# Optimization experiments

Measured on AMD Instinct MI355X. Metric: run time of the kernel, lower is better.

Reference implementation:

```python
import jax, jax.numpy as jnp
import numpy as np
import math

B, T, D, H = 4, 2048, 1024, 16
DH = D // H

def setup_inputs() -> dict:
    key = jax.random.key(0)
    ks = jax.random.split(key, 5)
    scale = 1.0 / math.sqrt(D)
    x = jax.random.normal(ks[0], (B, T, D), dtype=jnp.float32)
    Wq = jax.random.normal(ks[1], (D, D), dtype=jnp.float32) * scale
    Wk = jax.random.normal(ks[2], (D, D), dtype=jnp.float32) * scale
    Wv = jax.random.normal(ks[3], (D, D), dtype=jnp.float32) * scale
    Wo = jax.random.normal(ks[4], (D, D), dtype=jnp.float32) * scale
    mask = jnp.tril(jnp.ones((T, T), dtype=jnp.int32))  # causal, 1=keep
    return {"x": x, "mask": mask, "Wq": Wq, "Wk": Wk, "Wv": Wv, "Wo": Wo}

def reference(x, mask, Wq, Wk, Wv, Wo):
    Bx, Tx, Dx = x.shape
    # nn.Linear(bias=False): y = x @ W.T
    q = (x @ Wq.T).reshape(Bx, Tx, H, DH).transpose(0, 2, 1, 3)  # [B,H,T,dh]
    k = (x @ Wk.T).reshape(Bx, Tx, H, DH).transpose(0, 2, 1, 3)
    v = (x @ Wv.T).reshape(Bx, Tx, H, DH).transpose(0, 2, 1, 3)
    scores = jnp.einsum('bhqd,bhkd->bhqk', q, k) / math.sqrt(DH)
    m = mask[None, None, :, :]  # [1,1,T,T]
    scores = scores + (m == 0).astype(scores.dtype) * -1e9
    attn = jax.nn.softmax(scores, axis=-1)  # stable (max-subtract) like original
    out = jnp.einsum('bhqk,bhkd->bhqd', attn, v)
    out = out.transpose(0, 2, 1, 3).reshape(Bx, Tx, Dx)
    return out @ Wo.T
```

## Files before the change

kernel.cpp:

```cpp
#include <hip/hip_runtime.h>
#include <stdint.h>

#define B_  4
#define T_  2048
#define D_  1024
#define H_  16
#define DH_ 64

typedef unsigned short u16;
typedef __attribute__((ext_vector_type(8))) short bf16x8;
typedef __attribute__((ext_vector_type(8))) unsigned short u16x8;
typedef __attribute__((ext_vector_type(4))) unsigned short u16x4;
typedef __attribute__((ext_vector_type(4))) float f32x4;

#define NT_ ((size_t)B_ * T_ * D_)
#define QSCALE 0.18033688011112043f

__device__ __forceinline__ u16 f2bf(float f) {
    union { float f; uint32_t u; } v; v.f = f;
    uint32_t r = v.u + 0x7FFFu + ((v.u >> 16) & 1u);
    return (u16)(r >> 16);
}

__device__ __forceinline__ uint32_t pack2(float lo, float hi) {
    union { float f; uint32_t u; } a, b; a.f = lo; b.f = hi;
    return __builtin_amdgcn_perm(b.u, a.u, 0x07060302u);
}

__device__ __forceinline__ void gl2lds16(const u16* g, u16* l) {
    __builtin_amdgcn_global_load_lds(
        (const __attribute__((address_space(1))) unsigned int*)g,
        (__attribute__((address_space(3))) unsigned int*)l,
        16, 0, 0);
}

#define VMCNT(n) asm volatile("s_waitcnt vmcnt(" #n ")" ::: "memory")
#define SB0()    __builtin_amdgcn_sched_barrier(0)

__device__ __forceinline__ bf16x8 ldsrd(const u16* base, int row, int ks,
                                        int lq, int swzr) {
    int off = row * 128 + ks * 64 + lq * 16;
    return *(const bf16x8*)((const char*)base + (off ^ swzr));
}

__global__ __launch_bounds__(256) void cvt_x_kernel(
    const float* __restrict__ src, u16* __restrict__ dst, int n8)
{
    int i = blockIdx.x * 256 + threadIdx.x;
    if (i >= n8) return;
    f32x4 a = ((const f32x4*)src)[2 * i];
    f32x4 b = ((const f32x4*)src)[2 * i + 1];
    u16x8 o;
    o[0]=f2bf(a[0]); o[1]=f2bf(a[1]); o[2]=f2bf(a[2]); o[3]=f2bf(a[3]);
    o[4]=f2bf(b[0]); o[5]=f2bf(b[1]); o[6]=f2bf(b[2]); o[7]=f2bf(b[3]);
    ((u16x8*)dst)[i] = o;
}

__global__ __launch_bounds__(256) void cvt_w_kernel(
    const float* __restrict__ w0, const float* __restrict__ w1,
    const float* __restrict__ w2, const float* __restrict__ w3,
    u16* __restrict__ dst)
{
    const float* src = (blockIdx.y == 0) ? w0 : (blockIdx.y == 1) ? w1
                     : (blockIdx.y == 2) ? w2 : w3;
    u16* d = dst + (size_t)blockIdx.y * (D_ * D_);
    int i = blockIdx.x * 256 + threadIdx.x;
    f32x4 a = ((const f32x4*)src)[2 * i];
    f32x4 b = ((const f32x4*)src)[2 * i + 1];
    u16x8 o;
    o[0]=f2bf(a[0]); o[1]=f2bf(a[1]); o[2]=f2bf(a[2]); o[3]=f2bf(a[3]);
    o[4]=f2bf(b[0]); o[5]=f2bf(b[1]); o[6]=f2bf(b[2]); o[7]=f2bf(b[3]);
    ((u16x8*)d)[i] = o;
}

template<int OUT_MODE>
__global__ __launch_bounds__(512) void gemm8_kernel(
    const u16* __restrict__ X, const u16* __restrict__ W,
    void* __restrict__ C, int M, int N, int K)
{
    __shared__ __align__(16) u16 Ab2[2][256 * 64];
    __shared__ __align__(16) u16 Bb2[2][192 * 64];

    const int tid  = threadIdx.x;
    const int wave = tid >> 6;
    const int lane = tid & 63;
    const int lq = lane >> 4, lm = lane & 15;
    const int wm = wave >> 2;
    const int wn = wave & 3;

    const int xcd = (int)blockIdx.x & 7;
    const int idx = (int)blockIdx.x >> 3;
    const int m0 = (((xcd & 3) << 3) + (idx & 7)) << 8;
    const int n0 = (((xcd >> 2) << 3) + (idx >> 3)) * 192;

    const int srow = wave * 8 + (lane >> 3);
    const int scol = ((lane & 7) ^ (lane >> 3)) << 3;
    const u16* gA = X + (size_t)(m0 + srow) * K + scol;
    const u16* gB = W + (size_t)(n0 + srow) * K + scol;
    const size_t rK64 = (size_t)64 * K;

    const int swzr = (lm & 7) << 4;

    f32x4 acc[8][3] = {};
    bf16x8 afA[2][2], afB[2][2];
    bf16x8 bqA[3][2], bqB[3][2];
    const int NT = K >> 6;

    gl2lds16(gA,            (u16*)Ab2[0] + wave * 512);
    gl2lds16(gA + rK64,     (u16*)Ab2[0] + 4096  + wave * 512);
    gl2lds16(gA + 2 * rK64, (u16*)Ab2[0] + 8192  + wave * 512);
    gl2lds16(gA + 3 * rK64, (u16*)Ab2[0] + 12288 + wave * 512);
    gl2lds16(gB,            (u16*)Bb2[0] + wave * 512);
    gl2lds16(gB + rK64,     (u16*)Bb2[0] + 4096  + wave * 512);
    gl2lds16(gB + 2 * rK64, (u16*)Bb2[0] + 8192  + wave * 512);
    gl2lds16(gB + 64,            (u16*)Bb2[1] + wave * 512);
    gl2lds16(gB + 64 + rK64,     (u16*)Bb2[1] + 4096  + wave * 512);
    gl2lds16(gB + 64 + 2 * rK64, (u16*)Bb2[1] + 8192  + wave * 512);
    VMCNT(3);
    __builtin_amdgcn_s_barrier();
#pragma unroll
    for (int i2 = 0; i2 < 2; ++i2)
#pragma unroll
        for (int ks = 0; ks < 2; ++ks)
            afA[i2][ks] = ldsrd(Ab2[0], wm * 128 + i2 * 16 + lm, ks, lq, swzr);
#pragma unroll
    for (int j = 0; j < 3; ++j)
#pragma unroll
        for (int ks = 0; ks < 2; ++ks)
            bqA[j][ks] = ldsrd(Bb2[0], wn * 48 + j * 16 + lm, ks, lq, swzr);

    auto tile_body = [&](int t, bf16x8 (&bqU)[3][2], bf16x8 (&bqF)[3][2])
        __attribute__((always_inline)) -> void {
        const u16* Ac = Ab2[t & 1];
        const u16* An = Ab2[(t + 1) & 1];
        const u16* Bn = Bb2[(t + 1) & 1];
        u16* Abn = (u16*)Ab2[(t + 1) & 1];
        u16* Bbc = (u16*)Bb2[t & 1];
        const bool stA = (t + 1 < NT);
        const bool stB = (t + 2 < NT);
        const u16* gAs = gA + (size_t)(t + 1) * 64;
        const u16* gBs = gB + (size_t)(t + 2) * 64;

#define MFMA_PH(Q, AF, BQ)                                                  \
        __builtin_amdgcn_s_setprio(1);                                      \
        _Pragma("unroll")                                                   \
        for (int ks = 0; ks < 2; ++ks)                                      \
            _Pragma("unroll")                                               \
            for (int i2 = 0; i2 < 2; ++i2)                                  \
                _Pragma("unroll")                                           \
                for (int j = 0; j < 3; ++j)                                 \
                    acc[2 * (Q) + i2][j] =                                  \
                        __builtin_amdgcn_mfma_f32_16x16x32_bf16(            \
                            AF[i2][ks], BQ[j][ks], acc[2 * (Q) + i2][j],    \
                            0, 0, 0);                                       \
        __builtin_amdgcn_s_setprio(0);

#define RD_AF(SET, P, BASE)                                                 \
        _Pragma("unroll")                                                   \
        for (int i2 = 0; i2 < 2; ++i2)                                      \
            _Pragma("unroll")                                               \
            for (int ks = 0; ks < 2; ++ks)                                  \
                SET[i2][ks] = ldsrd(BASE,                                   \
                    wm * 128 + (2 * (P) + i2) * 16 + lm, ks, lq, swzr);

        RD_AF(afB, 1, Ac);
        if (stA) {
            gl2lds16(gAs,        Abn + wave * 512);
            gl2lds16(gAs + rK64, Abn + 4096 + wave * 512);
        }
        SB0(); __builtin_amdgcn_s_barrier(); SB0();
        MFMA_PH(0, afA, bqU); SB0();
        __builtin_amdgcn_s_barrier();

        RD_AF(afA, 2, Ac);
        if (stA) {
            gl2lds16(gAs + 2 * rK64, Abn + 8192  + wave * 512);
            gl2lds16(gAs + 3 * rK64, Abn + 12288 + wave * 512);
        }
        SB0(); __builtin_amdgcn_s_barrier(); SB0();
        MFMA_PH(1, afB, bqU); SB0();
        __builtin_amdgcn_s_barrier();

        RD_AF(afB, 3, Ac);
        if (stB) {
            gl2lds16(gBs,        Bbc + wave * 512);
            gl2lds16(gBs + rK64, Bbc + 4096 + wave * 512);
        }
        SB0(); __builtin_amdgcn_s_barrier(); SB0();
        MFMA_PH(2, afA, bqU); SB0();
        if (stB)      { VMCNT(2); }
        else if (stA) { VMCNT(0); }
        __builtin_amdgcn_s_barrier();

        if (stA) {
            RD_AF(afA, 0, An);
#pragma unroll
            for (int j = 0; j < 3; ++j)
#pragma unroll
                for (int ks = 0; ks < 2; ++ks)
                    bqF[j][ks] = ldsrd(Bn, wn * 48 + j * 16 + lm, ks, lq, swzr);
        }
        if (stB)
            gl2lds16(gBs + 2 * rK64, Bbc + 8192 + wave * 512);
        SB0(); __builtin_amdgcn_s_barrier(); SB0();
        MFMA_PH(3, afB, bqU); SB0();
        __builtin_amdgcn_s_barrier();
#undef RD_AF
#undef MFMA_PH
    };

#pragma unroll 1
    for (int tt = 0; tt < NT; tt += 2) {
        tile_body(tt,     bqA, bqB);
        tile_body(tt + 1, bqB, bqA);
    }

#pragma unroll
    for (int i = 0; i < 8; ++i)
#pragma unroll
        for (int j = 0; j < 3; ++j) {
            int rowb = m0 + wm * 128 + i * 16 + lq * 4;
            int col  = n0 + wn * 48 + j * 16 + lm;
            if (OUT_MODE == 2) {
#pragma unroll
                for (int r = 0; r < 4; ++r)
                    ((float*)C)[(size_t)(rowb + r) * N + col] = acc[i][j][r];
            } else {
                u16* Qp = (u16*)C;
                int region = col >> 10;
                int colr = col & 1023;
                if (region == 0) {
#pragma unroll
                    for (int r = 0; r < 4; ++r)
                        Qp[(size_t)(rowb + r) * D_ + colr] = f2bf(acc[i][j][r] * QSCALE);
                } else if (region == 1) {
#pragma unroll
                    for (int r = 0; r < 4; ++r)
                        (Qp + NT_)[(size_t)(rowb + r) * D_ + colr] = f2bf(acc[i][j][r]);
                } else {
                    int b = rowb >> 11, tt2 = rowb & (T_ - 1);
                    u16x4 pk;
#pragma unroll
                    for (int r = 0; r < 4; ++r) pk[r] = f2bf(acc[i][j][r]);
                    *(u16x4*)((Qp + 2 * NT_) + ((size_t)b * D_ + colr) * T_ + tt2) = pk;
                }
            }
        }
}

__global__ __launch_bounds__(256) void gemm_bt_kernel(
    const u16* __restrict__ X, const u16* __restrict__ W,
    float* __restrict__ C, int M, int N, int K)
{
    __shared__ __align__(16) u16 As[128 * 64];
    __shared__ __align__(16) u16 Bs[128 * 64];

    const int tid  = threadIdx.x;
    const int wave = tid >> 6;
    const int lane = tid & 63;
    const int lq = lane >> 4;
    const int lm = lane & 15;
    const int m0 = blockIdx.x * 128;
    const int n0 = blockIdx.y * 128;
    const int wm = (wave & 1) * 64;
    const int wn = (wave >> 1) * 64;

    f32x4 acc[4][4] = {};

    const int r0 = wave * 32 + (lane >> 3);
    const int c0 = (lane & 7) * 8;
    const u16* gA = X + (size_t)(m0 + r0) * K + c0;
    const u16* gB = W + (size_t)(n0 + r0) * K + c0;
    u16* lA = As + wave * 32 * 64;
    u16* lB = Bs + wave * 32 * 64;

    for (int k0 = 0; k0 < K; k0 += 64) {
#pragma unroll
        for (int p = 0; p < 4; ++p) {
            gl2lds16(gA + (size_t)p * 8 * K + k0, lA + p * 8 * 64);
            gl2lds16(gB + (size_t)p * 8 * K + k0, lB + p * 8 * 64);
        }
        __syncthreads();
#pragma unroll
        for (int ks = 0; ks < 2; ++ks) {
            bf16x8 af[4], bfr[4];
#pragma unroll
            for (int t = 0; t < 4; ++t)
                af[t] = *(const bf16x8*)(As + (wm + t * 16 + lm) * 64 + ks * 32 + lq * 8);
#pragma unroll
            for (int t = 0; t < 4; ++t)
                bfr[t] = *(const bf16x8*)(Bs + (wn + t * 16 + lm) * 64 + ks * 32 + lq * 8);
#pragma unroll
            for (int i = 0; i < 4; ++i)
#pragma unroll
                for (int j = 0; j < 4; ++j)
                    acc[i][j] = __builtin_amdgcn_mfma_f32_16x16x32_bf16(
                        af[i], bfr[j], acc[i][j], 0, 0, 0);
        }
        __syncthreads();
    }

#pragma unroll
    for (int i = 0; i < 4; ++i)
#pragma unroll
        for (int j = 0; j < 4; ++j) {
            int rowb = m0 + wm + i * 16 + lq * 4;
            int col  = n0 + wn + j * 16 + lm;
#pragma unroll
            for (int r = 0; r < 4; ++r)
                C[(size_t)(rowb + r) * N + col] = acc[i][j][r];
        }
}

__global__ __launch_bounds__(128) void attn_kernel(
    const u16* __restrict__ Qg, const u16* __restrict__ Kg,
    const u16* __restrict__ Vtg, u16* __restrict__ Og)
{
    __shared__ __align__(16) u16 Pl[2 * 64 * 40];

    const int tid  = threadIdx.x;
    const int wave = tid >> 6;
    const int lane = tid & 63;
    const int lq = lane >> 4, lm = lane & 15;
    const int id = blockIdx.x;
    const int xs = id & 7;
    const int bh = xs + 8 * ((id >> 3) & 7);
    const int qj = 31 - (id >> 6);
    const int b = bh >> 4, h = bh & 15;

    const size_t batchoff = (size_t)b * T_ * D_;
    const size_t headoff  = (size_t)h * DH_;
    const size_t vbase    = (size_t)bh * DH_ * T_;

    u16* pw = Pl + wave * 64 * 40;

    const int qw  = qj * 64;
    const int ktd = qj >> 1;
    const int odd = qj & 1;

    bf16x8 aq[4][2];
#pragma unroll
    for (int qf = 0; qf < 4; ++qf) {
        const u16* qrow = Qg + batchoff + (size_t)(qw + qf * 16 + lm) * D_ + headoff;
        aq[qf][0] = *(const bf16x8*)(qrow + lq * 8);
        aq[qf][1] = *(const bf16x8*)(qrow + 32 + lq * 8);
    }

    f32x4 oaccT[4][4] = {};
    float l_lane[4] = {0.f, 0.f, 0.f, 0.f};

#pragma unroll 1
    for (int kt = wave; kt <= ktd; kt += 2) {
        const bool diag = (kt == ktd);
        const int ksmax = diag ? (odd ? 3 : 1) : 3;

#pragma unroll
        for (int c = 0; c < 4; ++c) {
            if (c <= ksmax) {
#pragma unroll
                for (int t = 0; t < 2; ++t) {
                    const int mt = 2 * c + t;
                    const u16* krow = Kg + batchoff
                        + (size_t)(kt * 128 + mt * 16 + lm) * D_ + headoff;
                    bf16x8 kf0 = *(const bf16x8*)(krow + lq * 8);
                    bf16x8 kf1 = *(const bf16x8*)(krow + 32 + lq * 8);
                    f32x4 s[4];
#pragma unroll
                    for (int qf = 0; qf < 4; ++qf) {
                        s[qf] = f32x4{0.f, 0.f, 0.f, 0.f};
                        s[qf] = __builtin_amdgcn_mfma_f32_16x16x32_bf16(
                            kf0, aq[qf][0], s[qf], 0, 0, 0);
                        s[qf] = __builtin_amdgcn_mfma_f32_16x16x32_bf16(
                            kf1, aq[qf][1], s[qf], 0, 0, 0);
                    }
                    if (diag) {
                        int keyb = kt * 128 + mt * 16 + lq * 4;
#pragma unroll
                        for (int qf = 0; qf < 4; ++qf) {
                            int query = qw + qf * 16 + lm;
#pragma unroll
                            for (int r = 0; r < 4; ++r)
                                if (keyb + r > query) s[qf][r] = -1e9f;
                        }
                    }
#pragma unroll
                    for (int qf = 0; qf < 4; ++qf) {
                        float p0 = __builtin_amdgcn_exp2f(s[qf][0]);
                        float p1 = __builtin_amdgcn_exp2f(s[qf][1]);
                        float p2 = __builtin_amdgcn_exp2f(s[qf][2]);
                        float p3 = __builtin_amdgcn_exp2f(s[qf][3]);
                        l_lane[qf] += (p0 + p1) + (p2 + p3);
                        uint2 d; d.x = pack2(p0, p1); d.y = pack2(p2, p3);
                        *(uint2*)(pw + (qf * 16 + lm) * 40 + t * 16 + lq * 4) = d;
                    }
                }

                bf16x8 pf[4];
#pragma unroll
                for (int qf = 0; qf < 4; ++qf)
                    pf[qf] = *(const bf16x8*)(pw + (qf * 16 + lm) * 40 + lq * 8);
#pragma unroll
                for (int mo = 0; mo < 4; ++mo) {
                    const u16* vrow = Vtg + vbase
                        + (size_t)(mo * 16 + lm) * T_ + kt * 128 + c * 32;
                    bf16x8 vf = *(const bf16x8*)(vrow + lq * 8);
#pragma unroll
                    for (int qf = 0; qf < 4; ++qf)
                        oaccT[qf][mo] = __builtin_amdgcn_mfma_f32_16x16x32_bf16(
                            vf, pf[qf], oaccT[qf][mo], 0, 0, 0);
                }
            }
        }
    }

    float* Cf = (float*)Pl;
    const int cswz = (lane ^ (lane >> 3)) * 4;
    __syncthreads();
    if (wave == 1) {
#pragma unroll
        for (int qf = 0; qf < 2; ++qf)
#pragma unroll
            for (int mo = 0; mo < 4; ++mo)
                *(f32x4*)&Cf[(qf * 4 + mo) * 256 + cswz] = oaccT[qf][mo];
#pragma unroll
        for (int qf = 0; qf < 4; ++qf)
            Cf[2048 + qf * 64 + lane] = l_lane[qf];
    }
    __syncthreads();
    if (wave == 0) {
#pragma unroll
        for (int qf = 0; qf < 2; ++qf)
#pragma unroll
            for (int mo = 0; mo < 4; ++mo) {
                f32x4 o = *(const f32x4*)&Cf[(qf * 4 + mo) * 256 + cswz];
#pragma unroll
                for (int r = 0; r < 4; ++r) oaccT[qf][mo][r] += o[r];
            }
#pragma unroll
        for (int qf = 0; qf < 4; ++qf) l_lane[qf] += Cf[2048 + qf * 64 + lane];
    }
    __syncthreads();
    if (wave == 1) {
#pragma unroll
        for (int qf = 2; qf < 4; ++qf)
#pragma unroll
            for (int mo = 0; mo < 4; ++mo)
                *(f32x4*)&Cf[((qf - 2) * 4 + mo) * 256 + cswz] = oaccT[qf][mo];
    }
    __syncthreads();
    if (wave == 0) {
#pragma unroll
        for (int qf = 2; qf < 4; ++qf)
#pragma unroll
            for (int mo = 0; mo < 4; ++mo) {
                f32x4 o = *(const f32x4*)&Cf[((qf - 2) * 4 + mo) * 256 + cswz];
#pragma unroll
                for (int r = 0; r < 4; ++r) oaccT[qf][mo][r] += o[r];
            }
#pragma unroll
        for (int qf = 0; qf < 4; ++qf) {
            float l = l_lane[qf];
            l += __shfl_xor(l, 16, 64);
            l += __shfl_xor(l, 32, 64);
            float inv = 1.0f / l;
            int row = qw + qf * 16 + lm;
            u16* obase = Og + batchoff + (size_t)row * D_ + headoff;
#pragma unroll
            for (int mo = 0; mo < 4; ++mo) {
                uint2 d;
                d.x = pack2(oaccT[qf][mo][0] * inv, oaccT[qf][mo][1] * inv);
                d.y = pack2(oaccT[qf][mo][2] * inv, oaccT[qf][mo][3] * inv);
                *(uint2*)(obase + mo * 16 + lq * 4) = d;
            }
        }
    }
}

extern "C" void kernel_launch(void* const* d_in, const int* in_sizes, int n_in,
                              void* d_out, int out_size, void* d_ws, size_t ws_size,
                              hipStream_t stream)
{
    const float* x  = (const float*)d_in[0];
    const float* Wq = (const float*)d_in[2];
    const float* Wk = (const float*)d_in[3];
    const float* Wv = (const float*)d_in[4];
    const float* Wo = (const float*)d_in[5];

    const size_t DD = (size_t)D_ * D_;
    u16* Qb  = (u16*)d_ws;
    u16* Kb  = Qb + NT_;
    u16* Vb  = Kb + NT_;
    u16* Ob  = Vb + NT_;
    u16* xb  = Ob + NT_;
    u16* wb  = xb + NT_;

    const int M = B_ * T_;

    cvt_x_kernel<<<dim3((int)(NT_ / 8 / 256)), 256, 0, stream>>>(x, xb, (int)(NT_ / 8));
    cvt_w_kernel<<<dim3((int)(DD / 8 / 256), 4), 256, 0, stream>>>(Wq, Wk, Wv, Wo, wb);

    gemm8_kernel<3><<<dim3((M / 256) * (3 * D_ / 192)), 512, 0, stream>>>(
        xb, wb, Qb, M, 3 * D_, D_);

    attn_kernel<<<dim3(2048), 128, 0, stream>>>(Qb, Kb, Vb, Ob);

    gemm_bt_kernel<<<dim3(M / 128, D_ / 128), 256, 0, stream>>>(
        Ob, wb + 3 * DD, (float*)d_out, M, D_, D_);
}
```

Measured before the change: 267.8 us.

## Flatten attention KV loop and double-buffer K fragments in registers

Replaces the nested kt/c loop with a flattened iteration count processed by an always-inlined body, unrolled twice with ping-pong K register buffers. The next step's K fragments are prefetched while the current step's QK MFMAs, exp and PV MFMAs run. V fragments are loaded at the start of each step, hiding global-load latency behind compute. This costs more VGPRs, which may reduce occupancy. It also relies on the per-wave step count always being even.

```diff
diff --git a/kernel.cpp b/kernel.cpp
--- a/kernel.cpp
+++ b/kernel.cpp
@@ -337,6 +337,7 @@
     const int qw  = qj * 64;
     const int ktd = qj >> 1;
     const int odd = qj & 1;
+    const int cmax_d = odd ? 3 : 1;
 
     bf16x8 aq[4][2];
 #pragma unroll
@@ -349,68 +350,94 @@
     f32x4 oaccT[4][4] = {};
     float l_lane[4] = {0.f, 0.f, 0.f, 0.f};
 
-#pragma unroll 1
-    for (int kt = wave; kt <= ktd; kt += 2) {
-        const bool diag = (kt == ktd);
-        const int ksmax = diag ? (odd ? 3 : 1) : 3;
-
-#pragma unroll
-        for (int c = 0; c < 4; ++c) {
-            if (c <= ksmax) {
-#pragma unroll
-                for (int t = 0; t < 2; ++t) {
-                    const int mt = 2 * c + t;
-                    const u16* krow = Kg + batchoff
-                        + (size_t)(kt * 128 + mt * 16 + lm) * D_ + headoff;
-                    bf16x8 kf0 = *(const bf16x8*)(krow + lq * 8);
-                    bf16x8 kf1 = *(const bf16x8*)(krow + 32 + lq * 8);
-                    f32x4 s[4];
-#pragma unroll
-                    for (int qf = 0; qf < 4; ++qf) {
-                        s[qf] = f32x4{0.f, 0.f, 0.f, 0.f};
-                        s[qf] = __builtin_amdgcn_mfma_f32_16x16x32_bf16(
-                            kf0, aq[qf][0], s[qf], 0, 0, 0);
-                        s[qf] = __builtin_amdgcn_mfma_f32_16x16x32_bf16(
-                            kf1, aq[qf][1], s[qf], 0, 0, 0);
-                    }
-                    if (diag) {
-                        int keyb = kt * 128 + mt * 16 + lq * 4;
-#pragma unroll
-                        for (int qf = 0; qf < 4; ++qf) {
-                            int query = qw + qf * 16 + lm;
-#pragma unroll
-                            for (int r = 0; r < 4; ++r)
-                                if (keyb + r > query) s[qf][r] = -1e9f;
-                        }
-                    }
-#pragma unroll
-                    for (int qf = 0; qf < 4; ++qf) {
-                        float p0 = __builtin_amdgcn_exp2f(s[qf][0]);
-                        float p1 = __builtin_amdgcn_exp2f(s[qf][1]);
-                        float p2 = __builtin_amdgcn_exp2f(s[qf][2]);
-                        float p3 = __builtin_amdgcn_exp2f(s[qf][3]);
-                        l_lane[qf] += (p0 + p1) + (p2 + p3);
-                        uint2 d; d.x = pack2(p0, p1); d.y = pack2(p2, p3);
-                        *(uint2*)(pw + (qf * 16 + lm) * 40 + t * 16 + lq * 4) = d;
-                    }
-                }
-
-                bf16x8 pf[4];
-#pragma unroll
-                for (int qf = 0; qf < 4; ++qf)
-                    pf[qf] = *(const bf16x8*)(pw + (qf * 16 + lm) * 40 + lq * 8);
-#pragma unroll
-                for (int mo = 0; mo < 4; ++mo) {
-                    const u16* vrow = Vtg + vbase
-                        + (size_t)(mo * 16 + lm) * T_ + kt * 128 + c * 32;
-                    bf16x8 vf = *(const bf16x8*)(vrow + lq * 8);
-#pragma unroll
-                    for (int qf = 0; qf < 4; ++qf)
-                        oaccT[qf][mo] = __builtin_amdgcn_mfma_f32_16x16x32_bf16(
-                            vf, pf[qf], oaccT[qf][mo], 0, 0, 0);
+    const u16* Kb_lane = Kg + batchoff + headoff + (size_t)lm * D_ + lq * 8;
+    const u16* Vb_lane = Vtg + vbase + (size_t)lm * T_ + lq * 8;
+
+    int total = 0;
+    for (int k = wave; k <= ktd; k += 2)
+        total += (k == ktd) ? (cmax_d + 1) : 4;
+
+    int kt = wave, c = 0;
+    bf16x8 kA[4], kB[4];
+    {
+        const u16* kr0 = Kb_lane + ((size_t)(kt * 128) << 10);
+        kA[0] = *(const bf16x8*)(kr0);
+        kA[1] = *(const bf16x8*)(kr0 + 32);
+        kA[2] = *(const bf16x8*)(kr0 + 16 * D_);
+        kA[3] = *(const bf16x8*)(kr0 + 16 * D_ + 32);
+    }
+
+    auto body = [&](bf16x8 (&kc)[4], bf16x8 (&kn)[4])
+        __attribute__((always_inline)) -> void {
+        const int ckt = kt, cc = c;
+        int nkt = ckt, nc = cc + 1;
+        const int cmax = (ckt == ktd) ? cmax_d : 3;
+        if (nc > cmax) { nkt = ckt + 2; nc = 0; }
+        const int kb = ckt * 128 + cc * 32;
+
+        bf16x8 vf[4];
+#pragma unroll
+        for (int mo = 0; mo < 4; ++mo)
+            vf[mo] = *(const bf16x8*)(Vb_lane + (size_t)mo * 16 * T_ + kb);
+
+        if (nkt <= ktd) {
+            const u16* kr0 = Kb_lane + ((size_t)(nkt * 128 + nc * 32) << 10);
+            kn[0] = *(const bf16x8*)(kr0);
+            kn[1] = *(const bf16x8*)(kr0 + 32);
+            kn[2] = *(const bf16x8*)(kr0 + 16 * D_);
+            kn[3] = *(const bf16x8*)(kr0 + 16 * D_ + 32);
+        }
+
+#pragma unroll
+        for (int qf = 0; qf < 4; ++qf) {
+            f32x4 s0 = {0.f, 0.f, 0.f, 0.f}, s1 = {0.f, 0.f, 0.f, 0.f};
+            s0 = __builtin_amdgcn_mfma_f32_16x16x32_bf16(kc[0], aq[qf][0], s0, 0, 0, 0);
+            s0 = __builtin_amdgcn_mfma_f32_16x16x32_bf16(kc[1], aq[qf][1], s0, 0, 0, 0);
+            s1 = __builtin_amdgcn_mfma_f32_16x16x32_bf16(kc[2], aq[qf][0], s1, 0, 0, 0);
+            s1 = __builtin_amdgcn_mfma_f32_16x16x32_bf16(kc[3], aq[qf][1], s1, 0, 0, 0);
+            if (ckt == ktd) {
+                int query = qw + qf * 16 + lm;
+                int kb0 = kb + lq * 4;
+#pragma unroll
+                for (int r = 0; r < 4; ++r) {
+                    if (kb0 + r > query)      s0[r] = -1e9f;
+                    if (kb0 + 16 + r > query) s1[r] = -1e9f;
                 }
             }
-        }
+            float p00 = __builtin_amdgcn_exp2f(s0[0]);
+            float p01 = __builtin_amdgcn_exp2f(s0[1]);
+            float p02 = __builtin_amdgcn_exp2f(s0[2]);
+            float p03 = __builtin_amdgcn_exp2f(s0[3]);
+            float p10 = __builtin_amdgcn_exp2f(s1[0]);
+            float p11 = __builtin_amdgcn_exp2f(s1[1]);
+            float p12 = __builtin_amdgcn_exp2f(s1[2]);
+            float p13 = __builtin_amdgcn_exp2f(s1[3]);
+            l_lane[qf] += ((p00 + p01) + (p02 + p03)) + ((p10 + p11) + (p12 + p13));
+            uint2 d0, d1;
+            d0.x = pack2(p00, p01); d0.y = pack2(p02, p03);
+            d1.x = pack2(p10, p11); d1.y = pack2(p12, p13);
+            *(uint2*)(pw + (qf * 16 + lm) * 40 + lq * 4)      = d0;
+            *(uint2*)(pw + (qf * 16 + lm) * 40 + 16 + lq * 4) = d1;
+        }
+
+        bf16x8 pf[4];
+#pragma unroll
+        for (int qf = 0; qf < 4; ++qf)
+            pf[qf] = *(const bf16x8*)(pw + (qf * 16 + lm) * 40 + lq * 8);
+#pragma unroll
+        for (int mo = 0; mo < 4; ++mo)
+#pragma unroll
+            for (int qf = 0; qf < 4; ++qf)
+                oaccT[qf][mo] = __builtin_amdgcn_mfma_f32_16x16x32_bf16(
+                    vf[mo], pf[qf], oaccT[qf][mo], 0, 0, 0);
+
+        kt = nkt; c = nc;
+    };
+
+#pragma unroll 1
+    for (int it = 0; it < total; it += 2) {
+        body(kA, kB);
+        body(kB, kA);
     }
 
     float* Cf = (float*)Pl;
```

Measured after the change: 276.3 us. +3.2%, slower.

## Replace output projection GEMM with double-buffered 8-wave pipelined kernel

Applied to the files above, without the earlier changes.

The simple 128x128 output-projection GEMM, which loads a tile and then computes with full barriers, is replaced by a 256x128-tile, 512-thread kernel. The new kernel double-buffers A and B in LDS with swizzled layouts and interleaves global-to-LDS loads with MFMA phases. Blocks are remapped across XCDs for L2 locality, and s_setprio is raised around the MFMA groups, including those in the attention kernel. This aims to hide memory latency in the final GEMM, at the cost of more complex barrier and vmcnt scheduling and a larger LDS footprint.

```diff
diff --git a/kernel.cpp b/kernel.cpp
--- a/kernel.cpp
+++ b/kernel.cpp
@@ -248,64 +248,150 @@
         }
 }
 
-__global__ __launch_bounds__(256) void gemm_bt_kernel(
+__global__ __launch_bounds__(512) void gemm8o_kernel(
     const u16* __restrict__ X, const u16* __restrict__ W,
-    float* __restrict__ C, int M, int N, int K)
+    float* __restrict__ C)
 {
-    __shared__ __align__(16) u16 As[128 * 64];
-    __shared__ __align__(16) u16 Bs[128 * 64];
-
+    __shared__ __align__(16) u16 Ab2[2][256 * 64];
+    __shared__ __align__(16) u16 Bb2[2][128 * 64];
+
+    const int K = 1024, N = 1024;
     const int tid  = threadIdx.x;
     const int wave = tid >> 6;
     const int lane = tid & 63;
-    const int lq = lane >> 4;
-    const int lm = lane & 15;
-    const int m0 = blockIdx.x * 128;
-    const int n0 = blockIdx.y * 128;
-    const int wm = (wave & 1) * 64;
-    const int wn = (wave >> 1) * 64;
-
-    f32x4 acc[4][4] = {};
-
-    const int r0 = wave * 32 + (lane >> 3);
-    const int c0 = (lane & 7) * 8;
-    const u16* gA = X + (size_t)(m0 + r0) * K + c0;
-    const u16* gB = W + (size_t)(n0 + r0) * K + c0;
-    u16* lA = As + wave * 32 * 64;
-    u16* lB = Bs + wave * 32 * 64;
-
-    for (int k0 = 0; k0 < K; k0 += 64) {
-#pragma unroll
-        for (int p = 0; p < 4; ++p) {
-            gl2lds16(gA + (size_t)p * 8 * K + k0, lA + p * 8 * 64);
-            gl2lds16(gB + (size_t)p * 8 * K + k0, lB + p * 8 * 64);
-        }
-        __syncthreads();
-#pragma unroll
-        for (int ks = 0; ks < 2; ++ks) {
-            bf16x8 af[4], bfr[4];
-#pragma unroll
-            for (int t = 0; t < 4; ++t)
-                af[t] = *(const bf16x8*)(As + (wm + t * 16 + lm) * 64 + ks * 32 + lq * 8);
-#pragma unroll
-            for (int t = 0; t < 4; ++t)
-                bfr[t] = *(const bf16x8*)(Bs + (wn + t * 16 + lm) * 64 + ks * 32 + lq * 8);
-#pragma unroll
-            for (int i = 0; i < 4; ++i)
-#pragma unroll
-                for (int j = 0; j < 4; ++j)
-                    acc[i][j] = __builtin_amdgcn_mfma_f32_16x16x32_bf16(
-                        af[i], bfr[j], acc[i][j], 0, 0, 0);
-        }
-        __syncthreads();
-    }
-
-#pragma unroll
-    for (int i = 0; i < 4; ++i)
-#pragma unroll
-        for (int j = 0; j < 4; ++j) {
-            int rowb = m0 + wm + i * 16 + lq * 4;
-            int col  = n0 + wn + j * 16 + lm;
+    const int lq = lane >> 4, lm = lane & 15;
+    const int wm = wave >> 2;
+    const int wn = wave & 3;
+
+    const int xcd = (int)blockIdx.x & 7;
+    const int idx = (int)blockIdx.x >> 3;
+    const int m0 = (((xcd & 3) << 3) + (idx & 7)) << 8;
+    const int n0 = (((xcd >> 2) << 2) + (idx >> 3)) << 7;
+
+    const int srow = wave * 8 + (lane >> 3);
+    const int scol = ((lane & 7) ^ (lane >> 3)) << 3;
+    const u16* gA = X + (size_t)(m0 + srow) * K + scol;
+    const u16* gB = W + (size_t)(n0 + srow) * K + scol;
+    const size_t rK64 = (size_t)64 * K;
+
+    const int swzr = (lm & 7) << 4;
+
+    f32x4 acc[8][2] = {};
+    bf16x8 afA[2][2], afB[2][2];
+    bf16x8 bqA[2][2], bqB[2][2];
+    const int NT = 16;
+
+    gl2lds16(gA,            (u16*)Ab2[0] + wave * 512);
+    gl2lds16(gA + rK64,     (u16*)Ab2[0] + 4096  + wave * 512);
+    gl2lds16(gA + 2 * rK64, (u16*)Ab2[0] + 8192  + wave * 512);
+    gl2lds16(gA + 3 * rK64, (u16*)Ab2[0] + 12288 + wave * 512);
+    gl2lds16(gB,            (u16*)Bb2[0] + wave * 512);
+    gl2lds16(gB + rK64,     (u16*)Bb2[0] + 4096  + wave * 512);
+    gl2lds16(gB + 64,            (u16*)Bb2[1] + wave * 512);
+    gl2lds16(gB + 64 + rK64,     (u16*)Bb2[1] + 4096  + wave * 512);
+    VMCNT(2);
+    __builtin_amdgcn_s_barrier();
+#pragma unroll
+    for (int i2 = 0; i2 < 2; ++i2)
+#pragma unroll
+        for (int ks = 0; ks < 2; ++ks)
+            afA[i2][ks] = ldsrd(Ab2[0], wm * 128 + i2 * 16 + lm, ks, lq, swzr);
+#pragma unroll
+    for (int j = 0; j < 2; ++j)
+#pragma unroll
+        for (int ks = 0; ks < 2; ++ks)
+            bqA[j][ks] = ldsrd(Bb2[0], wn * 32 + j * 16 + lm, ks, lq, swzr);
+
+    auto tile_body = [&](int t, bf16x8 (&bqU)[2][2], bf16x8 (&bqF)[2][2])
+        __attribute__((always_inline)) -> void {
+        const u16* Ac = Ab2[t & 1];
+        const u16* An = Ab2[(t + 1) & 1];
+        const u16* Bn = Bb2[(t + 1) & 1];
+        u16* Abn = (u16*)Ab2[(t + 1) & 1];
+        u16* Bbc = (u16*)Bb2[t & 1];
+        const bool stA = (t + 1 < NT);
+        const bool stB = (t + 2 < NT);
+        const u16* gAs = gA + (size_t)(t + 1) * 64;
+        const u16* gBs = gB + (size_t)(t + 2) * 64;
+
+#define MFMA_PHO(Q, AF, BQ)                                                 \
+        __builtin_amdgcn_s_setprio(1);                                      \
+        _Pragma("unroll")                                                   \
+        for (int ks = 0; ks < 2; ++ks)                                      \
+            _Pragma("unroll")                                               \
+            for (int i2 = 0; i2 < 2; ++i2)                                  \
+                _Pragma("unroll")                                           \
+                for (int j = 0; j < 2; ++j)                                 \
+                    acc[2 * (Q) + i2][j] =                                  \
+                        __builtin_amdgcn_mfma_f32_16x16x32_bf16(            \
+                            AF[i2][ks], BQ[j][ks], acc[2 * (Q) + i2][j],    \
+                            0, 0, 0);                                       \
+        __builtin_amdgcn_s_setprio(0);
+
+#define RD_AFO(SET, P, BASE)                                                \
+        _Pragma("unroll")                                                   \
+        for (int i2 = 0; i2 < 2; ++i2)                                      \
+            _Pragma("unroll")                                               \
+            for (int ks = 0; ks < 2; ++ks)                                  \
+                SET[i2][ks] = ldsrd(BASE,                                   \
+                    wm * 128 + (2 * (P) + i2) * 16 + lm, ks, lq, swzr);
+
+        RD_AFO(afB, 1, Ac);
+        if (stA) {
+            gl2lds16(gAs,        Abn + wave * 512);
+            gl2lds16(gAs + rK64, Abn + 4096 + wave * 512);
+        }
+        SB0(); __builtin_amdgcn_s_barrier(); SB0();
+        MFMA_PHO(0, afA, bqU); SB0();
+        __builtin_amdgcn_s_barrier();
+
+        RD_AFO(afA, 2, Ac);
+        if (stA) {
+            gl2lds16(gAs + 2 * rK64, Abn + 8192  + wave * 512);
+            gl2lds16(gAs + 3 * rK64, Abn + 12288 + wave * 512);
+        }
+        SB0(); __builtin_amdgcn_s_barrier(); SB0();
+        MFMA_PHO(1, afB, bqU); SB0();
+        __builtin_amdgcn_s_barrier();
+
+        RD_AFO(afB, 3, Ac);
+        if (stB)
+            gl2lds16(gBs, Bbc + wave * 512);
+        SB0(); __builtin_amdgcn_s_barrier(); SB0();
+        MFMA_PHO(2, afA, bqU); SB0();
+        if (stB)      { VMCNT(1); }
+        else if (stA) { VMCNT(0); }
+        __builtin_amdgcn_s_barrier();
+
+        if (stA) {
+            RD_AFO(afA, 0, An);
+#pragma unroll
+            for (int j = 0; j < 2; ++j)
+#pragma unroll
+                for (int ks = 0; ks < 2; ++ks)
+                    bqF[j][ks] = ldsrd(Bn, wn * 32 + j * 16 + lm, ks, lq, swzr);
+        }
+        if (stB)
+            gl2lds16(gBs + rK64, Bbc + 4096 + wave * 512);
+        SB0(); __builtin_amdgcn_s_barrier(); SB0();
+        MFMA_PHO(3, afB, bqU); SB0();
+        __builtin_amdgcn_s_barrier();
+#undef RD_AFO
+#undef MFMA_PHO
+    };
+
+#pragma unroll 1
+    for (int tt = 0; tt < NT; tt += 2) {
+        tile_body(tt,     bqA, bqB);
+        tile_body(tt + 1, bqB, bqA);
+    }
+
+#pragma unroll
+    for (int i = 0; i < 8; ++i)
+#pragma unroll
+        for (int j = 0; j < 2; ++j) {
+            int rowb = m0 + wm * 128 + i * 16 + lq * 4;
+            int col  = n0 + wn * 32 + j * 16 + lm;
 #pragma unroll
             for (int r = 0; r < 4; ++r)
                 C[(size_t)(rowb + r) * N + col] = acc[i][j][r];
@@ -365,6 +451,7 @@
                     bf16x8 kf0 = *(const bf16x8*)(krow + lq * 8);
                     bf16x8 kf1 = *(const bf16x8*)(krow + 32 + lq * 8);
                     f32x4 s[4];
+                    __builtin_amdgcn_s_setprio(1);
 #pragma unroll
                     for (int qf = 0; qf < 4; ++qf) {
                         s[qf] = f32x4{0.f, 0.f, 0.f, 0.f};
@@ -373,6 +460,7 @@
                         s[qf] = __builtin_amdgcn_mfma_f32_16x16x32_bf16(
                             kf1, aq[qf][1], s[qf], 0, 0, 0);
                     }
+                    __builtin_amdgcn_s_setprio(0);
                     if (diag) {
                         int keyb = kt * 128 + mt * 16 + lq * 4;
 #pragma unroll
@@ -399,6 +487,7 @@
 #pragma unroll
                 for (int qf = 0; qf < 4; ++qf)
                     pf[qf] = *(const bf16x8*)(pw + (qf * 16 + lm) * 40 + lq * 8);
+                __builtin_amdgcn_s_setprio(1);
 #pragma unroll
                 for (int mo = 0; mo < 4; ++mo) {
                     const u16* vrow = Vtg + vbase
@@ -409,6 +498,7 @@
                         oaccT[qf][mo] = __builtin_amdgcn_mfma_f32_16x16x32_bf16(
                             vf, pf[qf], oaccT[qf][mo], 0, 0, 0);
                 }
+                __builtin_amdgcn_s_setprio(0);
             }
         }
     }
@@ -504,6 +594,5 @@
 
     attn_kernel<<<dim3(2048), 128, 0, stream>>>(Qb, Kb, Vb, Ob);
 
-    gemm_bt_kernel<<<dim3(M / 128, D_ / 128), 256, 0, stream>>>(
-        Ob, wb + 3 * DD, (float*)d_out, M, D_, D_);
-}
+    gemm8o_kernel<<<dim3(256), 512, 0, stream>>>(Ob, wb + 3 * DD, (float*)d_out);
+}
```

Result: no change. 269.3 us (+0.6%).
